# Kernel tuning notes

Measured on AMD Instinct MI355X. Metric: run time of the kernel, lower is better.

Reference implementation:

```python
import jax, jax.numpy as jnp
import numpy as np

HEADS = 16
GROUPS = 4


def setup_inputs() -> dict:
    key = jax.random.key(0)
    k1, k2, k3, k4 = jax.random.split(key, 4)
    d_model = 2048
    d_kv = d_model * GROUPS // HEADS  # 512
    x = jax.random.normal(k1, (2, 2048, d_model), dtype=jnp.float32)
    Wq = jax.random.normal(k2, (d_model, d_model), dtype=jnp.float32) * (d_model ** -0.5)
    Wk = jax.random.normal(k3, (d_kv, d_model), dtype=jnp.float32) * (d_model ** -0.5)
    Wv = jax.random.normal(k4, (d_kv, d_model), dtype=jnp.float32) * (d_model ** -0.5)
    return {"x": x, "Wq": Wq, "Wk": Wk, "Wv": Wv}


def reference(x, Wq, Wk, Wv):
    b, t, c = x.shape
    hd = c // HEADS  # head dim
    h2g = HEADS // GROUPS  # query heads per kv group
    # projections (nn.Linear applies x @ W.T)
    q = (x @ Wq.T).reshape(b, t, HEADS, hd).transpose(0, 2, 1, 3)   # [b,H,t,hd]
    k = (x @ Wk.T).reshape(b, t, GROUPS, hd).transpose(0, 2, 1, 3)  # [b,G,t,hd]
    v = (x @ Wv.T).reshape(b, t, GROUPS, hd).transpose(0, 2, 1, 3)  # [b,G,t,hd]
    # GQA broadcast: group query heads by kv group
    qg = q.reshape(b, GROUPS, h2g, t, hd)                            # [b,G,h2g,t,hd]
    scores = jnp.einsum('bghqd,bgkd->bghqk', qg, k) * (hd ** -0.5)  # [b,G,h2g,t,t]
    causal = jnp.tril(jnp.ones((t, t), dtype=bool))
    scores = jnp.where(causal, scores, -jnp.inf)
    weights = jax.nn.softmax(scores, axis=-1)
    out = jnp.einsum('bghqk,bgkd->bghqd', weights, v)               # [b,G,h2g,t,hd]
    out = out.reshape(b, HEADS, t, hd).transpose(0, 2, 1, 3).reshape(b, t, c)
    return out
```

## Files before the change

### kernel.cpp

```cpp
#include <hip/hip_runtime.h>
#include <hip/hip_bf16.h>

typedef __bf16 bf16x8 __attribute__((ext_vector_type(8)));
typedef float f32x4 __attribute__((ext_vector_type(4)));

#define MFMA16(a,b,c) __builtin_amdgcn_mfma_f32_16x16x32_bf16(a,b,c,0,0,0)
#define GLL16(src, dst) __builtin_amdgcn_global_load_lds( \
    (const __attribute__((address_space(1))) unsigned int*)(src), \
    (__attribute__((address_space(3))) unsigned int*)(dst), 16, 0, 0)
#define WAIT_VM(n)  asm volatile("s_waitcnt vmcnt(" #n ")")
#define BAR() __builtin_amdgcn_s_barrier()

__device__ inline unsigned int pack_bf16(float a, float b) {
    unsigned short ua = __builtin_bit_cast(unsigned short, (__bf16)a);
    unsigned short ub = __builtin_bit_cast(unsigned short, (__bf16)b);
    return ((unsigned int)ub << 16) | ua;
}
__device__ inline short bf_s(float v) {
    __bf16 b = (__bf16)v;
    return __builtin_bit_cast(short, b);
}

__global__ void cvt_all(const float* __restrict__ x,  const float* __restrict__ wq,
                        const float* __restrict__ wk, const float* __restrict__ wv,
                        __bf16* __restrict__ xb, __bf16* __restrict__ wb) {
    long i = (long)(blockIdx.x * blockDim.x + threadIdx.x) * 8;
    const float* src; __bf16* dst;
    if (i < 8388608)       { src = x  + i;              dst = xb + i; }
    else if (i < 12582912) { src = wq + (i - 8388608);  dst = wb + (i - 8388608); }
    else if (i < 13631488) { src = wk + (i - 12582912); dst = wb + (i - 12582912 + 4194304); }
    else                   { src = wv + (i - 13631488); dst = wb + (i - 13631488 + 5242880); }
    float4 a = *(const float4*)src;
    float4 b = *(const float4*)(src + 4);
    bf16x8 r;
    r[0] = (__bf16)a.x; r[1] = (__bf16)a.y; r[2] = (__bf16)a.z; r[3] = (__bf16)a.w;
    r[4] = (__bf16)b.x; r[5] = (__bf16)b.y; r[6] = (__bf16)b.z; r[7] = (__bf16)b.w;
    *(bf16x8*)dst = r;
}

__global__ __launch_bounds__(512, 2) void gemm_qkv(const __bf16* __restrict__ A,
                                                   const __bf16* __restrict__ B,
                                                   __bf16* __restrict__ Qb,
                                                   __bf16* __restrict__ Kf,
                                                   __bf16* __restrict__ Vf,
                                                   float qscale) {
    const int K = 2048;
    const int NT = 64;
    __shared__ __bf16 As[3 * 8192];
    __shared__ __bf16 Bs[3 * 8192];

    int tid = threadIdx.x;
    int wave = tid >> 6, lane = tid & 63;
    int quad = lane >> 4, l16 = lane & 15;
    int wr = wave >> 2, wc = wave & 3;

    int tm = blockIdx.x & 15, tn = blockIdx.x >> 4;

    const __bf16* Ab = A + (size_t)tm * 256 * K + (size_t)l16 * K + quad * 8;
    const __bf16* Bb = B + (size_t)tn * 256 * K + (size_t)l16 * K + quad * 8;

    auto stage = [&](int kt, int buf) {
#pragma unroll
        for (int r = 0; r < 2; ++r) {
            int mb = r * 8 + wave;
            GLL16(Ab + (size_t)mb * 16 * K + kt, As + buf * 8192 + mb * 512 + lane * 8);
            GLL16(Bb + (size_t)mb * 16 * K + kt, Bs + buf * 8192 + mb * 512 + lane * 8);
        }
    };

    f32x4 acc[8][4] = {};

    stage(0, 0);
    stage(32, 1);
    WAIT_VM(4);
    BAR();

    int cur = 0, nxt = 2;
    for (int t = 0; t < NT; ++t) {
        if (t + 2 < NT) stage((t + 2) << 5, nxt);

        const __bf16* Ac = As + cur * 8192;
        const __bf16* Bc = Bs + cur * 8192;
        bf16x8 a[8], b[4];
#pragma unroll
        for (int m = 0; m < 8; ++m)
            a[m] = *(const bf16x8*)(Ac + (wr * 8 + m) * 512 + lane * 8);
#pragma unroll
        for (int n = 0; n < 4; ++n)
            b[n] = *(const bf16x8*)(Bc + (wc * 4 + n) * 512 + lane * 8);
#pragma unroll
        for (int m = 0; m < 8; ++m)
#pragma unroll
            for (int n = 0; n < 4; ++n)
                acc[m][n] = MFMA16(a[m], b[n], acc[m][n]);

        if (t + 2 < NT)      WAIT_VM(4);
        else if (t + 1 < NT) WAIT_VM(0);
        BAR();
        cur = (cur == 2) ? 0 : cur + 1;
        nxt = (nxt == 2) ? 0 : nxt + 1;
    }

#pragma unroll
    for (int m = 0; m < 8; ++m) {
        int row0 = tm * 256 + wr * 128 + m * 16 + quad * 4;
        int bb = row0 >> 11, tok0 = row0 & 2047;
#pragma unroll
        for (int n = 0; n < 4; ++n) {
            int col = tn * 256 + wc * 64 + n * 16 + l16;
            if (tn < 8) {
#pragma unroll
                for (int r = 0; r < 4; ++r)
                    Qb[(size_t)(row0 + r) * 2048 + col] = (__bf16)(acc[m][n][r] * qscale);
            } else if (tn < 10) {
                int d_all = col - 2048;
                int g = d_all >> 7, dd = d_all & 127;
                int dt = dd >> 5, q4 = (dd >> 3) & 3, jj = dd & 7;
                int tb = tok0 >> 4, tl0 = tok0 & 15;
                __bf16* base = Kf + ((((size_t)(bb * 4 + g) * 128 + tb) * 4 + dt) * 512)
                               + (q4 * 16 + tl0) * 8 + jj;
#pragma unroll
                for (int r = 0; r < 4; ++r)
                    base[r * 8] = (__bf16)acc[m][n][r];
            } else {
                int d_all = col - 2560;
                int g = d_all >> 7, dd = d_all & 127;
                int nto = dd >> 4, dl = dd & 15;
                int ch = tok0 >> 6, kk = (tok0 >> 5) & 1;
                int q4v = (tok0 >> 3) & 3, jv0 = tok0 & 7;
                size_t off = ((((size_t)(bb * 4 + g) * 32 + ch) * 16) + nto * 2 + kk) * 512
                             + (q4v * 16 + dl) * 8 + jv0;
                short4 pk;
                pk.x = bf_s(acc[m][n][0]); pk.y = bf_s(acc[m][n][1]);
                pk.z = bf_s(acc[m][n][2]); pk.w = bf_s(acc[m][n][3]);
                *(short4*)(Vf + off) = pk;
            }
        }
    }
}

__global__ __launch_bounds__(256) void attn_mfma(const __bf16* __restrict__ Q,
                                                 const __bf16* __restrict__ Kf,
                                                 const __bf16* __restrict__ Vf,
                                                 float* __restrict__ O) {
    const int T = 2048, CM = 2048, HD = 128;
    __shared__ __bf16 Ks[2 * 8192];
    __shared__ __bf16 Vs[2 * 8192];
    __shared__ __bf16 Pl[8192];

    int tid = threadIdx.x;
    int wave = tid >> 6, lane = tid & 63;
    int quad = lane >> 4, l16 = lane & 15;

    int bg = blockIdx.x & 7;
    int slot = blockIdx.x >> 3;
    int qb = (slot < 32) ? (63 - slot) : (slot - 32);
    int b = bg >> 2, g = bg & 3;
    int h = g * 4 + wave;
    int q0 = qb * 32;

    bf16x8 qf[2][4];
    const __bf16* qbase = Q + (size_t)b * T * CM + (size_t)h * HD;
#pragma unroll
    for (int nt = 0; nt < 2; ++nt)
#pragma unroll
        for (int dt = 0; dt < 4; ++dt)
            qf[nt][dt] = *(const bf16x8*)(qbase + (size_t)(q0 + nt * 16 + l16) * CM
                                          + dt * 32 + quad * 8);

    const __bf16* kcb = Kf + (size_t)(b * 4 + g) * 262144;
    const __bf16* vcb = Vf + (size_t)(b * 4 + g) * 262144;

    float m_r[2] = {-1e30f, -1e30f}, l_r[2] = {0.f, 0.f};
    f32x4 o_acc[2][8] = {};
    __bf16* Pw = Pl + wave * 2048;

    auto stage_kv = [&](int ch, int buf) {
        const __bf16* kg = kcb + ch * 8192 + wave * 2048 + lane * 8;
        const __bf16* vg = vcb + ch * 8192 + wave * 2048 + lane * 8;
        __bf16* kl = Ks + buf * 8192 + wave * 2048 + lane * 8;
        __bf16* vl = Vs + buf * 8192 + wave * 2048 + lane * 8;
#pragma unroll
        for (int i = 0; i < 4; ++i) GLL16(kg + i * 512, kl + i * 512);
#pragma unroll
        for (int i = 0; i < 4; ++i) GLL16(vg + i * 512, vl + i * 512);
    };

    int nch = (qb >> 1) + 1;
    stage_kv(0, 0);
    for (int ch = 0; ch < nch; ++ch) {
        BAR();
        if (ch + 1 < nch) {
            stage_kv(ch + 1, (ch + 1) & 1);
            WAIT_VM(8);
        } else {
            WAIT_VM(0);
        }
        BAR();

        const __bf16* Kb = Ks + (ch & 1) * 8192;
        const __bf16* Vb = Vs + (ch & 1) * 8192;

        f32x4 st[2][4] = {};
        __builtin_amdgcn_s_setprio(1);
#pragma unroll
        for (int t = 0; t < 4; ++t)
#pragma unroll
            for (int dt = 0; dt < 4; ++dt) {
                bf16x8 kfv = *(const bf16x8*)(Kb + (t * 4 + dt) * 512 + lane * 8);
                st[0][t] = MFMA16(kfv, qf[0][dt], st[0][t]);
                st[1][t] = MFMA16(kfv, qf[1][dt], st[1][t]);
            }
        __builtin_amdgcn_s_setprio(0);

        bool diag = (ch == nch - 1);
        float alpha[2];
#pragma unroll
        for (int nt = 0; nt < 2; ++nt) {
            if (diag) {
                int qg = q0 + nt * 16 + l16;
#pragma unroll
                for (int t = 0; t < 4; ++t)
#pragma unroll
                    for (int r = 0; r < 4; ++r)
                        if (ch * 64 + t * 16 + quad * 4 + r > qg) st[nt][t][r] = -1e30f;
            }
            float cmax = -1e30f;
#pragma unroll
            for (int t = 0; t < 4; ++t)
                cmax = fmaxf(cmax, fmaxf(fmaxf(st[nt][t][0], st[nt][t][1]),
                                         fmaxf(st[nt][t][2], st[nt][t][3])));
            cmax = fmaxf(cmax, __shfl_xor(cmax, 16));
            cmax = fmaxf(cmax, __shfl_xor(cmax, 32));
            float mnew = fmaxf(m_r[nt], cmax);
            alpha[nt] = __expf(m_r[nt] - mnew);
            m_r[nt] = mnew;
            float ps = 0.f;
#pragma unroll
            for (int t = 0; t < 4; ++t) {
                float p0 = __expf(st[nt][t][0] - mnew);
                float p1 = __expf(st[nt][t][1] - mnew);
                float p2 = __expf(st[nt][t][2] - mnew);
                float p3 = __expf(st[nt][t][3] - mnew);
                ps += (p0 + p1) + (p2 + p3);
                int off = (nt * 2 + (t >> 1)) * 512 + ((t & 1) * 2 + (quad >> 1)) * 128
                          + l16 * 8 + (quad & 1) * 4;
                unsigned long long pk =
                    (unsigned long long)pack_bf16(p0, p1) |
                    ((unsigned long long)pack_bf16(p2, p3) << 32);
                *(unsigned long long*)(Pw + off) = pk;
            }
            ps += __shfl_xor(ps, 16);
            ps += __shfl_xor(ps, 32);
            l_r[nt] = l_r[nt] * alpha[nt] + ps;
        }

#pragma unroll
        for (int mt = 0; mt < 2; ++mt)
#pragma unroll
            for (int r = 0; r < 4; ++r) {
                float alr = __shfl(alpha[mt], quad * 4 + r);
#pragma unroll
                for (int nto = 0; nto < 8; ++nto)
                    o_acc[mt][nto][r] *= alr;
            }

        __builtin_amdgcn_s_setprio(1);
#pragma unroll
        for (int mt = 0; mt < 2; ++mt)
#pragma unroll
            for (int kk = 0; kk < 2; ++kk) {
                bf16x8 pf = *(const bf16x8*)(Pw + (mt * 2 + kk) * 512 + lane * 8);
#pragma unroll
                for (int nto = 0; nto < 8; ++nto) {
                    bf16x8 vf = *(const bf16x8*)(Vb + (nto * 2 + kk) * 512 + lane * 8);
                    o_acc[mt][nto] = MFMA16(pf, vf, o_acc[mt][nto]);
                }
            }
        __builtin_amdgcn_s_setprio(0);
    }

    float* obase = O + (size_t)b * T * CM + (size_t)h * HD;
#pragma unroll
    for (int mt = 0; mt < 2; ++mt) {
        float invl = 1.f / l_r[mt];
#pragma unroll
        for (int r = 0; r < 4; ++r) {
            float ir = __shfl(invl, quad * 4 + r);
            float* orow = obase + (size_t)(q0 + 16 * mt + quad * 4 + r) * CM;
#pragma unroll
            for (int nto = 0; nto < 8; ++nto)
                orow[nto * 16 + l16] = o_acc[mt][nto][r] * ir;
        }
    }
}

extern "C" void kernel_launch(void* const* d_in, const int* in_sizes, int n_in,
                              void* d_out, int out_size, void* d_ws, size_t ws_size,
                              hipStream_t stream) {
    const float* x  = (const float*)d_in[0];
    const float* Wq = (const float*)d_in[1];
    const float* Wk = (const float*)d_in[2];
    const float* Wv = (const float*)d_in[3];
    float* out = (float*)d_out;

    const float qscale = 0.08838834764831845f;

    __bf16* xb = (__bf16*)d_ws;
    __bf16* Wb = xb + 8388608;
    __bf16* Qb = Wb + 6291456;
    __bf16* Kfr = Qb + 8388608;
    __bf16* Vfr = Kfr + 2097152;

    cvt_all<<<7168, 256, 0, stream>>>(x, Wq, Wk, Wv, xb, Wb);
    gemm_qkv<<<192, 512, 0, stream>>>(xb, Wb, Qb, Kfr, Vfr, qscale);
    attn_mfma<<<512, 256, 0, stream>>>(Qb, Kfr, Vfr, out);
}
```

Before: 287.4 us.

## Shrink QKV GEMM tiles to 128x128 with double buffering for more blocks

The QKV projection GEMM moves from 256x256 tiles with a three-stage LDS pipeline and 8x4 MFMA accumulators per wave to 128x128 tiles with two-stage buffering and 2x4 accumulators. The grid grows from 192 to 768 blocks so that more blocks fill the GPU's compute units, and launch bounds are raised so more blocks can sit on each unit. The cost is less operand reuse per tile and twice the global and LDS traffic per FLOP. The pipeline also becomes shallower, with a __syncthreads each iteration and no explicit vmcnt waits.

```diff
diff --git a/kernel.cpp b/kernel.cpp
--- a/kernel.cpp
+++ b/kernel.cpp
@@ -38,81 +38,66 @@
     *(bf16x8*)dst = r;
 }
 
-__global__ __launch_bounds__(512, 2) void gemm_qkv(const __bf16* __restrict__ A,
+__global__ __launch_bounds__(512, 6) void gemm_qkv(const __bf16* __restrict__ A,
                                                    const __bf16* __restrict__ B,
                                                    __bf16* __restrict__ Qb,
                                                    __bf16* __restrict__ Kf,
                                                    __bf16* __restrict__ Vf,
                                                    float qscale) {
     const int K = 2048;
-    const int NT = 64;
-    __shared__ __bf16 As[3 * 8192];
-    __shared__ __bf16 Bs[3 * 8192];
+    __shared__ __bf16 As[2 * 4096];
+    __shared__ __bf16 Bs[2 * 4096];
 
     int tid = threadIdx.x;
     int wave = tid >> 6, lane = tid & 63;
     int quad = lane >> 4, l16 = lane & 15;
-    int wr = wave >> 2, wc = wave & 3;
-
-    int tm = blockIdx.x & 15, tn = blockIdx.x >> 4;
-
-    const __bf16* Ab = A + (size_t)tm * 256 * K + (size_t)l16 * K + quad * 8;
-    const __bf16* Bb = B + (size_t)tn * 256 * K + (size_t)l16 * K + quad * 8;
+    int wr = wave >> 1, wc = wave & 1;
+
+    int tm = blockIdx.x & 31, tn = blockIdx.x >> 5;
+
+    const __bf16* Abase = A + (size_t)tm * 128 * K + (size_t)l16 * K + quad * 8;
+    const __bf16* Bbase = B + (size_t)tn * 128 * K + (size_t)l16 * K + quad * 8;
+
+    f32x4 acc[2][4] = {};
 
     auto stage = [&](int kt, int buf) {
-#pragma unroll
-        for (int r = 0; r < 2; ++r) {
-            int mb = r * 8 + wave;
-            GLL16(Ab + (size_t)mb * 16 * K + kt, As + buf * 8192 + mb * 512 + lane * 8);
-            GLL16(Bb + (size_t)mb * 16 * K + kt, Bs + buf * 8192 + mb * 512 + lane * 8);
-        }
+        GLL16(Abase + (size_t)wave * 16 * K + kt, As + buf * 4096 + wave * 512 + lane * 8);
+        GLL16(Bbase + (size_t)wave * 16 * K + kt, Bs + buf * 4096 + wave * 512 + lane * 8);
     };
 
-    f32x4 acc[8][4] = {};
-
+    const int nk = K >> 5;
     stage(0, 0);
-    stage(32, 1);
-    WAIT_VM(4);
-    BAR();
-
-    int cur = 0, nxt = 2;
-    for (int t = 0; t < NT; ++t) {
-        if (t + 2 < NT) stage((t + 2) << 5, nxt);
-
-        const __bf16* Ac = As + cur * 8192;
-        const __bf16* Bc = Bs + cur * 8192;
-        bf16x8 a[8], b[4];
-#pragma unroll
-        for (int m = 0; m < 8; ++m)
-            a[m] = *(const bf16x8*)(Ac + (wr * 8 + m) * 512 + lane * 8);
+    for (int it = 0; it < nk; ++it) {
+        __syncthreads();
+        if (it + 1 < nk) stage((it + 1) << 5, (it + 1) & 1);
+        const __bf16* Ab = As + (it & 1) * 4096;
+        const __bf16* Bb = Bs + (it & 1) * 4096;
+        bf16x8 af[2], bfr[4];
+#pragma unroll
+        for (int m = 0; m < 2; ++m)
+            af[m] = *(const bf16x8*)(Ab + (wr * 2 + m) * 512 + lane * 8);
 #pragma unroll
         for (int n = 0; n < 4; ++n)
-            b[n] = *(const bf16x8*)(Bc + (wc * 4 + n) * 512 + lane * 8);
-#pragma unroll
-        for (int m = 0; m < 8; ++m)
+            bfr[n] = *(const bf16x8*)(Bb + (wc * 4 + n) * 512 + lane * 8);
+#pragma unroll
+        for (int m = 0; m < 2; ++m)
 #pragma unroll
             for (int n = 0; n < 4; ++n)
-                acc[m][n] = MFMA16(a[m], b[n], acc[m][n]);
-
-        if (t + 2 < NT)      WAIT_VM(4);
-        else if (t + 1 < NT) WAIT_VM(0);
-        BAR();
-        cur = (cur == 2) ? 0 : cur + 1;
-        nxt = (nxt == 2) ? 0 : nxt + 1;
+                acc[m][n] = MFMA16(af[m], bfr[n], acc[m][n]);
     }
 
 #pragma unroll
-    for (int m = 0; m < 8; ++m) {
-        int row0 = tm * 256 + wr * 128 + m * 16 + quad * 4;
+    for (int m = 0; m < 2; ++m) {
+        int row0 = tm * 128 + wr * 32 + m * 16 + quad * 4;
         int bb = row0 >> 11, tok0 = row0 & 2047;
 #pragma unroll
         for (int n = 0; n < 4; ++n) {
-            int col = tn * 256 + wc * 64 + n * 16 + l16;
-            if (tn < 8) {
+            int col = tn * 128 + wc * 64 + n * 16 + l16;
+            if (tn < 16) {
 #pragma unroll
                 for (int r = 0; r < 4; ++r)
                     Qb[(size_t)(row0 + r) * 2048 + col] = (__bf16)(acc[m][n][r] * qscale);
-            } else if (tn < 10) {
+            } else if (tn < 20) {
                 int d_all = col - 2048;
                 int g = d_all >> 7, dd = d_all & 127;
                 int dt = dd >> 5, q4 = (dd >> 3) & 3, jj = dd & 7;
@@ -313,6 +298,6 @@
     __bf16* Vfr = Kfr + 2097152;
 
     cvt_all<<<7168, 256, 0, stream>>>(x, Wq, Wk, Wv, xb, Wb);
-    gemm_qkv<<<192, 512, 0, stream>>>(xb, Wb, Qb, Kfr, Vfr, qscale);
+    gemm_qkv<<<768, 512, 0, stream>>>(xb, Wb, Qb, Kfr, Vfr, qscale);
     attn_mfma<<<512, 256, 0, stream>>>(Qb, Kfr, Vfr, out);
 }
```

Result: faster. 273.1 us (-5.0%).
